# Kernel tuning notes

Hardware: AMD Instinct MI355X
Metric: run time of the kernel (lower is better)

## Reference

```python
import jax, jax.numpy as jnp
import numpy as np

IN_FEATURES = 4096
OUT_FEATURES = 4096
K = 256
D = 8

def setup_inputs() -> dict:
    key = jax.random.key(0)
    k1, k2, k3 = jax.random.split(key, 3)
    x = jax.random.normal(k1, (4, 2048, IN_FEATURES), dtype=jnp.float32)
    codebook = jax.random.normal(k2, (K, D), dtype=jnp.float16)
    n_codes = OUT_FEATURES * IN_FEATURES // D  # 2,097,152
    indices = jax.random.randint(k3, (n_codes,), 0, K, dtype=jnp.int64)
    return {"x": x, "codebook": codebook, "indices": indices}

def reference(x, codebook, indices):
    orig_dtype = x.dtype
    x_fp16 = x.astype(jnp.float16)
    # Gather codes then reshape into the dense weight [out_features, in_features]
    W_q = codebook[indices].reshape(OUT_FEATURES, IN_FEATURES)  # fp16
    # F.linear: out = x @ W.T
    out = jnp.einsum('bsi,oi->bso', x_fp16, W_q)
    return out.astype(orig_dtype)
```

## Files before the change

### kernel.cpp

```cpp
#include <hip/hip_runtime.h>


typedef _Float16 f16;
typedef _Float16 f16x8 __attribute__((ext_vector_type(8)));
typedef float f32x4 __attribute__((ext_vector_type(4)));

#define KDIM 4096
#define NDIM 4096
#define MDIM 8192

struct Flags { int cb_mode; int x_bf16; int idx64; int pad; };

__device__ inline float bf16_to_f32(unsigned short w) {
    union { unsigned u; float f; } c; c.u = ((unsigned)w) << 16; return c.f;
}
__device__ inline unsigned short f32_to_bf16(float f) {
    union { float f; unsigned u; } c; c.f = f;
    unsigned r = c.u + 0x7FFFu + ((c.u >> 16) & 1u);
    return (unsigned short)(r >> 16);
}


__global__ __launch_bounds__(256) void crom_detect(const unsigned short* __restrict__ cbw,
                                                   const unsigned short* __restrict__ xw,
                                                   const unsigned* __restrict__ idxw,
                                                   Flags* __restrict__ flags) {
    __shared__ int cnt[4];
    const int t = threadIdx.x;
    if (t < 4) cnt[t] = 0;
    __syncthreads();
    int c_cb = 0, c_f32ok = 1, c_x = 0, c_z = 0;
    for (int j = 0; j < 8; ++j) {
        int e5 = (cbw[t * 8 + j] >> 10) & 31;
        c_cb += (e5 == 15) || (e5 == 16);
    }
    const float* cbf = (const float*)cbw;
    for (int j = 0; j < 4; ++j) {
        float v = cbf[t * 4 + j];
        if (!(__builtin_fabsf(v) < 1024.0f)) c_f32ok = 0;
        else { f16 h = (f16)v; if ((float)h != v) c_f32ok = 0; }
    }
    for (int j = 0; j < 8; ++j) {
        int e8 = (xw[t * 8 + j] >> 7) & 255;
        c_x += (e8 >= 115) && (e8 <= 131);
    }
    for (int j = 1; j < 8; j += 2) c_z += (idxw[t * 8 + j] == 0);
    atomicAdd(&cnt[0], c_cb);
    atomicAdd(&cnt[1], c_f32ok);
    atomicAdd(&cnt[2], c_x);
    atomicAdd(&cnt[3], c_z);
    __syncthreads();
    if (t == 0) {
        flags->cb_mode = (cnt[1] == 256) ? 2 : ((cnt[0] > 1300) ? 1 : 0);
        flags->x_bf16  = cnt[2] > 1600;
        flags->idx64   = cnt[3] > 512;
    }
}

__global__ __launch_bounds__(256) void crom_dequant(const void* __restrict__ idxraw,
                                                    const void* __restrict__ cbraw,
                                                    uint4* __restrict__ W,
                                                    const Flags* __restrict__ flags) {
    __shared__ __align__(16) f16 cbL[256 * 8];
    const int t = threadIdx.x;
    const int cb_mode = flags->cb_mode;
    if (cb_mode == 2) {
        const float* cf = (const float*)cbraw;
        f16x8 h;
        for (int j = 0; j < 8; ++j) h[j] = (f16)cf[t * 8 + j];
        *(f16x8*)&cbL[t * 8] = h;
    } else if (cb_mode == 1) {
        const unsigned short* cw = (const unsigned short*)cbraw;
        f16x8 h;
        for (int j = 0; j < 8; ++j) h[j] = (f16)bf16_to_f32(cw[t * 8 + j]);
        *(f16x8*)&cbL[t * 8] = h;
    } else {
        ((uint4*)cbL)[t] = ((const uint4*)cbraw)[t];
    }
    __syncthreads();
    int i = blockIdx.x * 256 + t;
    int code = flags->idx64 ? (int)((const long long*)idxraw)[i]
                            : ((const int*)idxraw)[i];
    W[i] = *(const uint4*)&cbL[code * 8];
}

__global__ __launch_bounds__(256) void crom_cvt_x(const void* __restrict__ X,
                                                  f16x8* __restrict__ Xh,
                                                  const Flags* __restrict__ flags) {
    int i = blockIdx.x * 256 + threadIdx.x;
    f16x8 h;
    if (flags->x_bf16) {
        ushort4 a = ((const ushort4*)X)[2 * i];
        ushort4 b = ((const ushort4*)X)[2 * i + 1];
        h[0] = (f16)bf16_to_f32(a.x); h[1] = (f16)bf16_to_f32(a.y);
        h[2] = (f16)bf16_to_f32(a.z); h[3] = (f16)bf16_to_f32(a.w);
        h[4] = (f16)bf16_to_f32(b.x); h[5] = (f16)bf16_to_f32(b.y);
        h[6] = (f16)bf16_to_f32(b.z); h[7] = (f16)bf16_to_f32(b.w);
    } else {
        float4 a = ((const float4*)X)[2 * i];
        float4 b = ((const float4*)X)[2 * i + 1];
        h[0] = (f16)a.x; h[1] = (f16)a.y; h[2] = (f16)a.z; h[3] = (f16)a.w;
        h[4] = (f16)b.x; h[5] = (f16)b.y; h[6] = (f16)b.z; h[7] = (f16)b.w;
    }
    Xh[i] = h;
}

__global__ __launch_bounds__(256) void crom_gemm(const f16* __restrict__ A,
                                                 const f16* __restrict__ B,
                                                 void* __restrict__ Cout,
                                                 const Flags* __restrict__ flags) {
    __shared__ __align__(16) f16 As[128 * 64];
    __shared__ __align__(16) f16 Bs[128 * 64];

    const int tid  = threadIdx.x;
    const int w    = tid >> 6;
    const int l    = tid & 63;
    const int m0   = blockIdx.y * 128;
    const int n0   = blockIdx.x * 128;
    const int wm   = (w >> 1) * 64;
    const int wn   = (w & 1) * 64;
    const int quad = l >> 4;
    const int lr   = l & 15;
    const int out_bf16 = flags->x_bf16;

    f32x4 acc[4][4] = {};

    for (int kb = 0; kb < KDIM / 64; ++kb) {
        const int k0 = kb * 64;
#pragma unroll
        for (int it = 0; it < 4; ++it) {
            int c   = it * 256 + w * 64 + l;
            int row = c >> 3;
            int sc  = (c & 7) ^ (row & 7);
            const f16* ga = A + (size_t)(m0 + row) * KDIM + k0 + sc * 8;
            const f16* gb = B + (size_t)(n0 + row) * KDIM + k0 + sc * 8;
            f16* la = &As[(size_t)(it * 256 + w * 64) * 8];
            f16* lb = &Bs[(size_t)(it * 256 + w * 64) * 8];
            __builtin_amdgcn_global_load_lds(
                (const __attribute__((address_space(1))) void*)ga,
                (__attribute__((address_space(3))) void*)la, 16, 0, 0);
            __builtin_amdgcn_global_load_lds(
                (const __attribute__((address_space(1))) void*)gb,
                (__attribute__((address_space(3))) void*)lb, 16, 0, 0);
        }
        __syncthreads();

#pragma unroll
        for (int ks = 0; ks < 2; ++ks) {
            f16x8 af[4], bf[4];
            const int gc = ks * 4 + quad;
            const int cc = gc ^ (lr & 7);
#pragma unroll
            for (int mt = 0; mt < 4; ++mt)
                af[mt] = *(const f16x8*)&As[(wm + mt * 16 + lr) * 64 + cc * 8];
#pragma unroll
            for (int nt = 0; nt < 4; ++nt)
                bf[nt] = *(const f16x8*)&Bs[(wn + nt * 16 + lr) * 64 + cc * 8];
#pragma unroll
            for (int mt = 0; mt < 4; ++mt)
#pragma unroll
                for (int nt = 0; nt < 4; ++nt)
                    acc[mt][nt] = __builtin_amdgcn_mfma_f32_16x16x32_f16(
                        af[mt], bf[nt], acc[mt][nt], 0, 0, 0);
        }
        __syncthreads();
    }

    if (out_bf16) {
        unsigned short* Cb = (unsigned short*)Cout;
#pragma unroll
        for (int mt = 0; mt < 4; ++mt)
#pragma unroll
            for (int nt = 0; nt < 4; ++nt) {
                int colg = n0 + wn + nt * 16 + lr;
#pragma unroll
                for (int r = 0; r < 4; ++r) {
                    int rowg = m0 + wm + mt * 16 + quad * 4 + r;
                    Cb[(size_t)rowg * NDIM + colg] = f32_to_bf16(acc[mt][nt][r]);
                }
            }
    } else {
        float* Cf = (float*)Cout;
#pragma unroll
        for (int mt = 0; mt < 4; ++mt)
#pragma unroll
            for (int nt = 0; nt < 4; ++nt) {
                int colg = n0 + wn + nt * 16 + lr;
#pragma unroll
                for (int r = 0; r < 4; ++r) {
                    int rowg = m0 + wm + mt * 16 + quad * 4 + r;
                    Cf[(size_t)rowg * NDIM + colg] = acc[mt][nt][r];
                }
            }
    }
}


__global__ __launch_bounds__(256) void crom_fused(const void* __restrict__ xraw,
                                                  const void* __restrict__ cbraw,
                                                  const void* __restrict__ idxraw,
                                                  void* __restrict__ outraw) {
    __shared__ __align__(16) f16 cbL[256 * 8];
    __shared__ __align__(16) f16 As[128 * 64];
    __shared__ __align__(16) f16 Bs[128 * 64];
    __shared__ int flagsL[4];

    const int t = threadIdx.x;
    {
        int c_cb = 0, c_f32ok = 1, c_x = 0, c_z = 0;
        const unsigned short* cbw = (const unsigned short*)cbraw;
        for (int j = 0; j < 8; ++j) {
            int e5 = (cbw[t * 8 + j] >> 10) & 31;
            c_cb += (e5 == 15) || (e5 == 16);
        }
        const float* cbf = (const float*)cbraw;
        for (int j = 0; j < 4; ++j) {
            float v = cbf[t * 4 + j];
            if (!(__builtin_fabsf(v) < 1024.0f)) c_f32ok = 0;
            else { f16 h = (f16)v; if ((float)h != v) c_f32ok = 0; }
        }
        const unsigned short* xw = (const unsigned short*)xraw;
        for (int j = 0; j < 8; ++j) {
            int e8 = (xw[t * 8 + j] >> 7) & 255;
            c_x += (e8 >= 115) && (e8 <= 131);
        }
        const unsigned* iw = (const unsigned*)idxraw;
        for (int j = 1; j < 8; j += 2) c_z += (iw[t * 8 + j] == 0);
        if (t < 4) flagsL[t] = 0;
        __syncthreads();
        atomicAdd(&flagsL[0], c_cb);
        atomicAdd(&flagsL[1], c_f32ok);
        atomicAdd(&flagsL[2], c_x);
        atomicAdd(&flagsL[3], c_z);
        __syncthreads();
    }
    const int cb_mode = (flagsL[1] == 256) ? 2 : ((flagsL[0] > 1300) ? 1 : 0);
    const int x_bf16  = flagsL[2] > 1600;
    const int idx64   = flagsL[3] > 512;

    if (cb_mode == 2) {
        const float* cf = (const float*)cbraw;
        f16x8 h;
        for (int j = 0; j < 8; ++j) h[j] = (f16)cf[t * 8 + j];
        *(f16x8*)&cbL[t * 8] = h;
    } else if (cb_mode == 1) {
        const unsigned short* cw = (const unsigned short*)cbraw;
        f16x8 h;
        for (int j = 0; j < 8; ++j) h[j] = (f16)bf16_to_f32(cw[t * 8 + j]);
        *(f16x8*)&cbL[t * 8] = h;
    } else {
        ((uint4*)cbL)[t] = ((const uint4*)cbraw)[t];
    }
    __syncthreads();

    const int m0 = blockIdx.y * 128;
    const int n0 = blockIdx.x * 128;
    const int w = t >> 6, l = t & 63, quad = l >> 4, lr = l & 15;
    const int wm = (w >> 1) * 64, wn = (w & 1) * 64;

    f32x4 acc[4][4] = {};

    for (int kb = 0; kb < KDIM / 64; ++kb) {
        const int k0 = kb * 64;
#pragma unroll
        for (int cc = 0; cc < 4; ++cc) {
            int c = cc * 256 + t, row = c >> 3, j = c & 7;
            int gc = j ^ (row & 7);
            f16x8 h;
            if (!x_bf16) {
                const float4* p = (const float4*)((const float*)xraw +
                                  (size_t)(m0 + row) * KDIM + k0 + gc * 8);
                float4 a = p[0], b = p[1];
                h[0] = (f16)a.x; h[1] = (f16)a.y; h[2] = (f16)a.z; h[3] = (f16)a.w;
                h[4] = (f16)b.x; h[5] = (f16)b.y; h[6] = (f16)b.z; h[7] = (f16)b.w;
            } else {
                const unsigned short* p = (const unsigned short*)xraw +
                                          (size_t)(m0 + row) * KDIM + k0 + gc * 8;
                ushort4 a = *(const ushort4*)p, b = *(const ushort4*)(p + 4);
                h[0] = (f16)bf16_to_f32(a.x); h[1] = (f16)bf16_to_f32(a.y);
                h[2] = (f16)bf16_to_f32(a.z); h[3] = (f16)bf16_to_f32(a.w);
                h[4] = (f16)bf16_to_f32(b.x); h[5] = (f16)bf16_to_f32(b.y);
                h[6] = (f16)bf16_to_f32(b.z); h[7] = (f16)bf16_to_f32(b.w);
            }
            *(f16x8*)&As[row * 64 + j * 8] = h;
        }
#pragma unroll
        for (int cc = 0; cc < 4; ++cc) {
            int c = cc * 256 + t, row = c >> 3, j = c & 7;
            int gc = j ^ (row & 7);
            int cpos = (n0 + row) * (KDIM / 8) + kb * 8 + gc;
            int code = idx64 ? (int)((const long long*)idxraw)[cpos]
                             : ((const int*)idxraw)[cpos];
            *(f16x8*)&Bs[row * 64 + j * 8] = *(const f16x8*)&cbL[code * 8];
        }
        __syncthreads();

#pragma unroll
        for (int ks = 0; ks < 2; ++ks) {
            f16x8 af[4], bf[4];
            int gc = ks * 4 + quad;
            int cc2 = gc ^ (lr & 7);
#pragma unroll
            for (int mt = 0; mt < 4; ++mt)
                af[mt] = *(const f16x8*)&As[(wm + mt * 16 + lr) * 64 + cc2 * 8];
#pragma unroll
            for (int nt = 0; nt < 4; ++nt)
                bf[nt] = *(const f16x8*)&Bs[(wn + nt * 16 + lr) * 64 + cc2 * 8];
#pragma unroll
            for (int mt = 0; mt < 4; ++mt)
#pragma unroll
                for (int nt = 0; nt < 4; ++nt)
                    acc[mt][nt] = __builtin_amdgcn_mfma_f32_16x16x32_f16(
                        af[mt], bf[nt], acc[mt][nt], 0, 0, 0);
        }
        __syncthreads();
    }

    if (x_bf16) {
        unsigned short* Cb = (unsigned short*)outraw;
#pragma unroll
        for (int mt = 0; mt < 4; ++mt)
#pragma unroll
            for (int nt = 0; nt < 4; ++nt) {
                int colg = n0 + wn + nt * 16 + lr;
#pragma unroll
                for (int r = 0; r < 4; ++r) {
                    int rowg = m0 + wm + mt * 16 + quad * 4 + r;
                    Cb[(size_t)rowg * NDIM + colg] = f32_to_bf16(acc[mt][nt][r]);
                }
            }
    } else {
        float* Cf = (float*)outraw;
#pragma unroll
        for (int mt = 0; mt < 4; ++mt)
#pragma unroll
            for (int nt = 0; nt < 4; ++nt) {
                int colg = n0 + wn + nt * 16 + lr;
#pragma unroll
                for (int r = 0; r < 4; ++r) {
                    int rowg = m0 + wm + mt * 16 + quad * 4 + r;
                    Cf[(size_t)rowg * NDIM + colg] = acc[mt][nt][r];
                }
            }
    }
}


extern "C" void kernel_launch(void* const* d_in, const int* in_sizes, int n_in,
                              void* d_out, int out_size, void* d_ws, size_t ws_size,
                              hipStream_t stream) {
    (void)in_sizes; (void)n_in; (void)out_size;
    const void* x   = d_in[0];
    const void* cb  = d_in[1];
    const void* idx = d_in[2];

    const size_t NEED = (size_t)96 * 1024 * 1024 + 4096;
    dim3 grid(NDIM / 128, MDIM / 128);

    if (ws_size >= NEED) {
        f16*   Wq    = (f16*)d_ws;
        f16*   Xh    = (f16*)((char*)d_ws + (size_t)32 * 1024 * 1024);
        Flags* flags = (Flags*)((char*)d_ws + (size_t)96 * 1024 * 1024);

        crom_detect<<<1, 256, 0, stream>>>((const unsigned short*)cb,
                                           (const unsigned short*)x,
                                           (const unsigned*)idx, flags);
        crom_dequant<<<2097152 / 256, 256, 0, stream>>>(idx, cb, (uint4*)Wq, flags);
        crom_cvt_x<<<(33554432 / 8) / 256, 256, 0, stream>>>(x, (f16x8*)Xh, flags);
        crom_gemm<<<grid, 256, 0, stream>>>(Xh, Wq, d_out, flags);
    } else {
        crom_fused<<<grid, 256, 0, stream>>>(x, cb, idx, d_out);
    }
}
```

Before: 550.5 us.

## Rewrite GEMM with 256x256 tiles, 8 waves, double-buffered LDS pipeline

Replaces the 128x128, 4-wave GEMM with a 256x256-tile, 512-thread kernel. It double-buffers A/B in LDS and issues half-tile async global-to-LDS loads in between MFMA quarter-blocks, using explicit vmcnt waits, barriers and setprio. It also adds a swizzled 1D block order for L2 locality and gives each wave more MFMA work per LDS fragment load. The costs are heavier register pressure from the larger accumulator and a 128KB LDS footprint, which limits occupancy.

```diff
diff --git a/kernel.cpp b/kernel.cpp
--- a/kernel.cpp
+++ b/kernel.cpp
@@ -105,90 +105,188 @@
     Xh[i] = h;
 }
 
-__global__ __launch_bounds__(256) void crom_gemm(const f16* __restrict__ A,
-                                                 const f16* __restrict__ B,
-                                                 void* __restrict__ Cout,
-                                                 const Flags* __restrict__ flags) {
-    __shared__ __align__(16) f16 As[128 * 64];
-    __shared__ __align__(16) f16 Bs[128 * 64];
+
+__device__ __forceinline__ void stage_A(const f16* __restrict__ A, f16* dstbuf,
+                                        int m0, int kt, int half, int w, int l) {
+#pragma unroll
+    for (int it = 0; it < 2; ++it) {
+        const int gb = it * 512 + w * 64;
+        const int g  = gb + l;
+        const int lrl = g >> 3, j = g & 7;
+        const int r  = ((lrl >> 6) << 7) + (half << 6) + (lrl & 63);
+        const int sc = j ^ (r & 7);
+        const f16* src = A + (size_t)(m0 + r) * KDIM + kt * 64 + sc * 8;
+        const int lrb = gb >> 3;
+        const int rb  = ((lrb >> 6) << 7) + (half << 6) + (lrb & 63);
+        __builtin_amdgcn_global_load_lds(
+            (const __attribute__((address_space(1))) void*)src,
+            (__attribute__((address_space(3))) void*)(dstbuf + rb * 64), 16, 0, 0);
+    }
+}
+
+__device__ __forceinline__ void stage_B(const f16* __restrict__ B, f16* dstbuf,
+                                        int n0, int kt, int half, int w, int l) {
+#pragma unroll
+    for (int it = 0; it < 2; ++it) {
+        const int gb = it * 512 + w * 64;
+        const int g  = gb + l;
+        const int lrl = g >> 3, j = g & 7;
+        const int r  = ((lrl >> 5) << 6) + (half << 5) + (lrl & 31);
+        const int sc = j ^ (r & 7);
+        const f16* src = B + (size_t)(n0 + r) * KDIM + kt * 64 + sc * 8;
+        const int lrb = gb >> 3;
+        const int rb  = ((lrb >> 5) << 6) + (half << 5) + (lrb & 31);
+        __builtin_amdgcn_global_load_lds(
+            (const __attribute__((address_space(1))) void*)src,
+            (__attribute__((address_space(3))) void*)(dstbuf + rb * 64), 16, 0, 0);
+    }
+}
+
+#define VMW(n) do { asm volatile("s_waitcnt vmcnt(" #n ")" ::: "memory"); \
+                    __builtin_amdgcn_sched_barrier(0); } while (0)
+
+#define LOAD_AF(Asb, QM)                                                      \
+    _Pragma("unroll")                                                         \
+    for (int mt = 0; mt < 4; ++mt) {                                          \
+        const int ro = (arow + (QM) * 64 + mt * 16) * 64;                     \
+        af[mt][0] = *(const f16x8*)&(Asb)[ro + c0];                           \
+        af[mt][1] = *(const f16x8*)&(Asb)[ro + c1];                           \
+    }
+
+#define LOAD_BF(Bsb, QN, bfx)                                                 \
+    _Pragma("unroll")                                                         \
+    for (int nt = 0; nt < 2; ++nt) {                                          \
+        const int ro = (brow + (QN) * 32 + nt * 16) * 64;                     \
+        bfx[nt][0] = *(const f16x8*)&(Bsb)[ro + c0];                          \
+        bfx[nt][1] = *(const f16x8*)&(Bsb)[ro + c1];                          \
+    }
+
+#define MFMA16(QM, QN, bfx)                                                   \
+    _Pragma("unroll")                                                         \
+    for (int ks = 0; ks < 2; ++ks)                                            \
+        _Pragma("unroll")                                                     \
+        for (int mt = 0; mt < 4; ++mt)                                        \
+            _Pragma("unroll")                                                 \
+            for (int nt = 0; nt < 2; ++nt)                                    \
+                acc[(QM) * 4 + mt][(QN) * 2 + nt] =                           \
+                    __builtin_amdgcn_mfma_f32_16x16x32_f16(                   \
+                        af[mt][ks], bfx[nt][ks],                              \
+                        acc[(QM) * 4 + mt][(QN) * 2 + nt], 0, 0, 0);
+
+#define BAR_MFMA(QM, QN, bfx, TAIL)                                           \
+    __builtin_amdgcn_s_barrier();                                             \
+    asm volatile("s_waitcnt lgkmcnt(0)" ::: "memory");                        \
+    __builtin_amdgcn_sched_barrier(0);                                        \
+    __builtin_amdgcn_s_setprio(1);                                            \
+    MFMA16(QM, QN, bfx);                                                      \
+    __builtin_amdgcn_s_setprio(0);                                            \
+    TAIL;                                                                     \
+    __builtin_amdgcn_s_barrier();
+
+__global__ __launch_bounds__(512, 2) void crom_gemm(const f16* __restrict__ A,
+                                                    const f16* __restrict__ B,
+                                                    void* __restrict__ Cout,
+                                                    const Flags* __restrict__ flags) {
+    __shared__ __align__(16) f16 As[2][256 * 64];
+    __shared__ __align__(16) f16 Bs[2][256 * 64];
 
     const int tid  = threadIdx.x;
     const int w    = tid >> 6;
     const int l    = tid & 63;
-    const int m0   = blockIdx.y * 128;
-    const int n0   = blockIdx.x * 128;
-    const int wm   = (w >> 1) * 64;
-    const int wn   = (w & 1) * 64;
     const int quad = l >> 4;
     const int lr   = l & 15;
+    const int wm   = w >> 2;
+    const int wn   = w & 3;
+
+    const int bid = blockIdx.x;
+    const int swz = (bid & 7) * 64 + (bid >> 3);
+    const int m0  = (swz >> 4) * 256;
+    const int n0  = (swz & 15) * 256;
+
+    const int c0 = (quad ^ (lr & 7)) * 8;
+    const int c1 = ((4 + quad) ^ (lr & 7)) * 8;
+    const int arow = wm * 128 + lr;
+    const int brow = wn * 64 + lr;
+
+    f32x4 acc[8][4] = {};
+    f16x8 af[4][2], bf0[2][2], bf1[2][2];
+
+    stage_A(A, As[0], m0, 0, 0, w, l);
+    stage_A(A, As[0], m0, 0, 1, w, l);
+    stage_B(B, Bs[0], n0, 0, 0, w, l);
+    stage_B(B, Bs[0], n0, 0, 1, w, l);
+    stage_A(A, As[1], m0, 1, 0, w, l);
+    stage_B(B, Bs[1], n0, 1, 0, w, l);
+    VMW(4);
+    __builtin_amdgcn_s_barrier();
+
+    for (int i = 0; i < 31; ++i) {
+        const int t0 = 2 * i;
+        LOAD_AF(As[0], 0); LOAD_BF(Bs[0], 0, bf0);
+        stage_A(A, As[1], m0, t0 + 1, 1, w, l);
+        BAR_MFMA(0, 0, bf0, );
+        LOAD_BF(Bs[0], 1, bf1);
+        stage_B(B, Bs[1], n0, t0 + 1, 1, w, l);
+        BAR_MFMA(0, 1, bf1, );
+        LOAD_AF(As[0], 1);
+        stage_A(A, As[0], m0, t0 + 2, 0, w, l);
+        BAR_MFMA(1, 0, bf0, );
+        stage_B(B, Bs[0], n0, t0 + 2, 0, w, l);
+        BAR_MFMA(1, 1, bf1, VMW(4));
+        LOAD_AF(As[1], 0); LOAD_BF(Bs[1], 0, bf0);
+        stage_A(A, As[0], m0, t0 + 2, 1, w, l);
+        BAR_MFMA(0, 0, bf0, );
+        LOAD_BF(Bs[1], 1, bf1);
+        stage_B(B, Bs[0], n0, t0 + 2, 1, w, l);
+        BAR_MFMA(0, 1, bf1, );
+        LOAD_AF(As[1], 1);
+        stage_A(A, As[1], m0, t0 + 3, 0, w, l);
+        BAR_MFMA(1, 0, bf0, );
+        stage_B(B, Bs[1], n0, t0 + 3, 0, w, l);
+        BAR_MFMA(1, 1, bf1, VMW(4));
+    }
+
+    LOAD_AF(As[0], 0); LOAD_BF(Bs[0], 0, bf0);
+    stage_A(A, As[1], m0, 63, 1, w, l);
+    BAR_MFMA(0, 0, bf0, );
+    LOAD_BF(Bs[0], 1, bf1);
+    stage_B(B, Bs[1], n0, 63, 1, w, l);
+    BAR_MFMA(0, 1, bf1, );
+    LOAD_AF(As[0], 1);
+    BAR_MFMA(1, 0, bf0, );
+    BAR_MFMA(1, 1, bf1, VMW(0));
+    LOAD_AF(As[1], 0); LOAD_BF(Bs[1], 0, bf0);
+    BAR_MFMA(0, 0, bf0, );
+    LOAD_BF(Bs[1], 1, bf1);
+    BAR_MFMA(0, 1, bf1, );
+    LOAD_AF(As[1], 1);
+    BAR_MFMA(1, 0, bf0, );
+    BAR_MFMA(1, 1, bf1, );
+
     const int out_bf16 = flags->x_bf16;
-
-    f32x4 acc[4][4] = {};
-
-    for (int kb = 0; kb < KDIM / 64; ++kb) {
-        const int k0 = kb * 64;
-#pragma unroll
-        for (int it = 0; it < 4; ++it) {
-            int c   = it * 256 + w * 64 + l;
-            int row = c >> 3;
-            int sc  = (c & 7) ^ (row & 7);
-            const f16* ga = A + (size_t)(m0 + row) * KDIM + k0 + sc * 8;
-            const f16* gb = B + (size_t)(n0 + row) * KDIM + k0 + sc * 8;
-            f16* la = &As[(size_t)(it * 256 + w * 64) * 8];
-            f16* lb = &Bs[(size_t)(it * 256 + w * 64) * 8];
-            __builtin_amdgcn_global_load_lds(
-                (const __attribute__((address_space(1))) void*)ga,
-                (__attribute__((address_space(3))) void*)la, 16, 0, 0);
-            __builtin_amdgcn_global_load_lds(
-                (const __attribute__((address_space(1))) void*)gb,
-                (__attribute__((address_space(3))) void*)lb, 16, 0, 0);
-        }
-        __syncthreads();
-
-#pragma unroll
-        for (int ks = 0; ks < 2; ++ks) {
-            f16x8 af[4], bf[4];
-            const int gc = ks * 4 + quad;
-            const int cc = gc ^ (lr & 7);
-#pragma unroll
-            for (int mt = 0; mt < 4; ++mt)
-                af[mt] = *(const f16x8*)&As[(wm + mt * 16 + lr) * 64 + cc * 8];
-#pragma unroll
-            for (int nt = 0; nt < 4; ++nt)
-                bf[nt] = *(const f16x8*)&Bs[(wn + nt * 16 + lr) * 64 + cc * 8];
-#pragma unroll
-            for (int mt = 0; mt < 4; ++mt)
-#pragma unroll
-                for (int nt = 0; nt < 4; ++nt)
-                    acc[mt][nt] = __builtin_amdgcn_mfma_f32_16x16x32_f16(
-                        af[mt], bf[nt], acc[mt][nt], 0, 0, 0);
-        }
-        __syncthreads();
-    }
-
     if (out_bf16) {
         unsigned short* Cb = (unsigned short*)Cout;
 #pragma unroll
-        for (int mt = 0; mt < 4; ++mt)
+        for (int mt = 0; mt < 8; ++mt)
 #pragma unroll
             for (int nt = 0; nt < 4; ++nt) {
-                int colg = n0 + wn + nt * 16 + lr;
+                const int colg = n0 + wn * 64 + nt * 16 + lr;
 #pragma unroll
                 for (int r = 0; r < 4; ++r) {
-                    int rowg = m0 + wm + mt * 16 + quad * 4 + r;
+                    const int rowg = m0 + wm * 128 + mt * 16 + quad * 4 + r;
                     Cb[(size_t)rowg * NDIM + colg] = f32_to_bf16(acc[mt][nt][r]);
                 }
             }
     } else {
         float* Cf = (float*)Cout;
 #pragma unroll
-        for (int mt = 0; mt < 4; ++mt)
+        for (int mt = 0; mt < 8; ++mt)
 #pragma unroll
             for (int nt = 0; nt < 4; ++nt) {
-                int colg = n0 + wn + nt * 16 + lr;
+                const int colg = n0 + wn * 64 + nt * 16 + lr;
 #pragma unroll
                 for (int r = 0; r < 4; ++r) {
-                    int rowg = m0 + wm + mt * 16 + quad * 4 + r;
+                    const int rowg = m0 + wm * 128 + mt * 16 + quad * 4 + r;
                     Cf[(size_t)rowg * NDIM + colg] = acc[mt][nt][r];
                 }
             }
@@ -201,8 +299,8 @@
                                                   const void* __restrict__ idxraw,
                                                   void* __restrict__ outraw) {
     __shared__ __align__(16) f16 cbL[256 * 8];
-    __shared__ __align__(16) f16 As[128 * 64];
-    __shared__ __align__(16) f16 Bs[128 * 64];
+    __shared__ __align__(16) f16 Asf[128 * 64];
+    __shared__ __align__(16) f16 Bsf[128 * 64];
     __shared__ int flagsL[4];
 
     const int t = threadIdx.x;
@@ -282,7 +380,7 @@
                 h[4] = (f16)bf16_to_f32(b.x); h[5] = (f16)bf16_to_f32(b.y);
                 h[6] = (f16)bf16_to_f32(b.z); h[7] = (f16)bf16_to_f32(b.w);
             }
-            *(f16x8*)&As[row * 64 + j * 8] = h;
+            *(f16x8*)&Asf[row * 64 + j * 8] = h;
         }
 #pragma unroll
         for (int cc = 0; cc < 4; ++cc) {
@@ -291,27 +389,27 @@
             int cpos = (n0 + row) * (KDIM / 8) + kb * 8 + gc;
             int code = idx64 ? (int)((const long long*)idxraw)[cpos]
                              : ((const int*)idxraw)[cpos];
-            *(f16x8*)&Bs[row * 64 + j * 8] = *(const f16x8*)&cbL[code * 8];
+            *(f16x8*)&Bsf[row * 64 + j * 8] = *(const f16x8*)&cbL[code * 8];
         }
         __syncthreads();
 
 #pragma unroll
         for (int ks = 0; ks < 2; ++ks) {
-            f16x8 af[4], bf[4];
+            f16x8 afv[4], bfv[4];
             int gc = ks * 4 + quad;
             int cc2 = gc ^ (lr & 7);
 #pragma unroll
             for (int mt = 0; mt < 4; ++mt)
-                af[mt] = *(const f16x8*)&As[(wm + mt * 16 + lr) * 64 + cc2 * 8];
+                afv[mt] = *(const f16x8*)&Asf[(wm + mt * 16 + lr) * 64 + cc2 * 8];
 #pragma unroll
             for (int nt = 0; nt < 4; ++nt)
-                bf[nt] = *(const f16x8*)&Bs[(wn + nt * 16 + lr) * 64 + cc2 * 8];
+                bfv[nt] = *(const f16x8*)&Bsf[(wn + nt * 16 + lr) * 64 + cc2 * 8];
 #pragma unroll
             for (int mt = 0; mt < 4; ++mt)
 #pragma unroll
                 for (int nt = 0; nt < 4; ++nt)
                     acc[mt][nt] = __builtin_amdgcn_mfma_f32_16x16x32_f16(
-                        af[mt], bf[nt], acc[mt][nt], 0, 0, 0);
+                        afv[mt], bfv[nt], acc[mt][nt], 0, 0, 0);
         }
         __syncthreads();
     }
@@ -355,7 +453,6 @@
     const void* idx = d_in[2];
 
     const size_t NEED = (size_t)96 * 1024 * 1024 + 4096;
-    dim3 grid(NDIM / 128, MDIM / 128);
 
     if (ws_size >= NEED) {
         f16*   Wq    = (f16*)d_ws;
@@ -367,8 +464,10 @@
                                            (const unsigned*)idx, flags);
         crom_dequant<<<2097152 / 256, 256, 0, stream>>>(idx, cb, (uint4*)Wq, flags);
         crom_cvt_x<<<(33554432 / 8) / 256, 256, 0, stream>>>(x, (f16x8*)Xh, flags);
-        crom_gemm<<<grid, 256, 0, stream>>>(Xh, Wq, d_out, flags);
-    } else {
+        crom_gemm<<<dim3((MDIM / 256) * (NDIM / 256)), dim3(512), 0, stream>>>(
+            Xh, Wq, d_out, flags);
+    } else {
+        dim3 grid(NDIM / 128, MDIM / 128);
         crom_fused<<<grid, 256, 0, stream>>>(x, cb, idx, d_out);
     }
 }
```

After: 471.5 us. -14.3%, faster.
